# Performance work log

Measured on AMD Instinct MI355X. Metric: run time of the kernel, lower is better.

The kernel has to match this reference:

```python
import jax, jax.numpy as jnp
import numpy as np

B, N = 262144, 32
NEG = -1e4  # acts as -inf: exp(NEG) == 0 in fp32, clean gradients (softmax weight 0)


def setup_inputs() -> dict:
    key = jax.random.key(0)
    k1, k2, k3 = jax.random.split(key, 3)
    scores = jax.random.normal(k1, (B, N), dtype=jnp.float32)
    ranks = jax.random.randint(k2, (B, N), 0, 32, dtype=jnp.int64)
    mask = jax.random.randint(k3, (B, N), 0, 2, dtype=jnp.int32).astype(bool)
    return {"scores": scores, "ranks": ranks, "mask": mask}


def reference(scores, ranks, mask):
    # n valid (non-padded) items per row
    n = jnp.sum(~mask, axis=1)                              # [B]
    # sort each row by rank, pushing padded entries to the end (stable sort,
    # matching per-row argsort over the valid subset in the original)
    sort_key = jnp.where(mask, N + 1, ranks)                # [B, N]
    order = jnp.argsort(sort_key, axis=1)                   # jnp argsort is stable
    s_sorted = jnp.take_along_axis(scores, order, axis=1)   # [B, N]

    pos = jnp.arange(N)
    valid = pos[None, :] < n[:, None]                       # first n slots hold valid scores
    s_m = jnp.where(valid, s_sorted, NEG)                   # padded -> effectively -inf

    # reverse cumulative logsumexp: rev_lse[k] = logsumexp(s_sorted[k:n])
    rev_lse = jax.lax.cumlogsumexp(s_m, axis=1, reverse=True)

    # original sums k = 0 .. n-2 of -(s_k - logsumexp(s_{k:}))
    term_mask = pos[None, :] < (n[:, None] - 1)
    per_row = -jnp.sum(jnp.where(term_mask, s_m - rev_lse, 0.0), axis=1)  # [B]

    use = n >= 2                                            # rows with < 2 valid are skipped
    per_row = jnp.where(use, per_row / jnp.maximum(n, 1).astype(per_row.dtype), 0.0)
    n_valid = jnp.sum(use)
    return jnp.sum(per_row) / jnp.maximum(n_valid, 1).astype(per_row.dtype)
```

## Files before the change

kernel.cpp:

```cpp
#include <hip/hip_runtime.h>
#include <cstdint>

#define TPB 256
#define LOG2E 1.4426950408889634f
#define LN2   0.69314718055994531f

__global__ __launch_bounds__(TPB, 4)
void pl_main(const float* __restrict__ scores,
             const int* __restrict__ ranks,
             const int* __restrict__ mask,
             float* __restrict__ partials,
             int B)
{
    const int tid = threadIdx.x;
    const int row = blockIdx.x * TPB + tid;

    __shared__ float eb[32 * TPB];

    float per_row = 0.0f, cnt = 0.0f;

    if (row < B) {
        const float4* sp = reinterpret_cast<const float4*>(scores) + (size_t)row * 8;
        const int4*   rp = reinterpret_cast<const int4*>(ranks)  + (size_t)row * 8;
        const int4*   mp = reinterpret_cast<const int4*>(mask)   + (size_t)row * 8;

        float4 sv[8];
        #pragma unroll
        for (int c = 0; c < 8; ++c) sv[c] = sp[c];

        unsigned K[32];
        int nm = 0;
        #pragma unroll
        for (int c = 0; c < 8; ++c) {
            const int4 rv = rp[c];
            const int4 qv = mp[c];
            const int j = c * 4;
            K[j+0] = (unsigned)((qv.x << 10) + (rv.x << 5) + (j+0));
            K[j+1] = (unsigned)((qv.y << 10) + (rv.y << 5) + (j+1));
            K[j+2] = (unsigned)((qv.z << 10) + (rv.z << 5) + (j+2));
            K[j+3] = (unsigned)((qv.w << 10) + (rv.w << 5) + (j+3));
            nm += (qv.x + qv.y) + (qv.z + qv.w);
        }
        const int n = 32 - nm;

        #pragma unroll
        for (int kk = 2; kk <= 32; kk <<= 1) {
            #pragma unroll
            for (int jj = kk >> 1; jj > 0; jj >>= 1) {
                #pragma unroll
                for (int i = 0; i < 32; ++i) {
                    const int l = i ^ jj;
                    if (l > i) {
                        const unsigned a = K[i], b = K[l];
                        const unsigned mn = a < b ? a : b;
                        const unsigned mh = a < b ? b : a;
                        if ((i & kk) == 0) { K[i] = mn; K[l] = mh; }
                        else               { K[i] = mh; K[l] = mn; }
                    }
                }
            }
        }

        float cm[8];
        #pragma unroll
        for (int c = 0; c < 8; ++c)
            cm[c] = fmaxf(fmaxf(sv[c].x, sv[c].y), fmaxf(sv[c].z, sv[c].w));
        const float mx = fmaxf(fmaxf(fmaxf(cm[0], cm[1]), fmaxf(cm[2], cm[3])),
                               fmaxf(fmaxf(cm[4], cm[5]), fmaxf(cm[6], cm[7])));
        const float nml = -mx * LOG2E;

        #pragma unroll
        for (int c = 0; c < 8; ++c) {
            const int j = c * 4;
            eb[(j+0)*TPB + tid] = __builtin_amdgcn_exp2f(__builtin_fmaf(sv[c].x, LOG2E, nml));
            eb[(j+1)*TPB + tid] = __builtin_amdgcn_exp2f(__builtin_fmaf(sv[c].y, LOG2E, nml));
            eb[(j+2)*TPB + tid] = __builtin_amdgcn_exp2f(__builtin_fmaf(sv[c].z, LOG2E, nml));
            eb[(j+3)*TPB + tid] = __builtin_amdgcn_exp2f(__builtin_fmaf(sv[c].w, LOG2E, nml));
        }

        float es[32];
        #pragma unroll
        for (int p = 0; p < 32; ++p)
            es[p] = eb[(K[p] & 31u) * TPB + tid];

        float t = 0.0f, lsum = 0.0f;
        #pragma unroll
        for (int g = 7; g >= 0; --g) {
            float pT = 1.0f, pE = 1.0f;
            #pragma unroll
            for (int q = 3; q >= 0; --q) {
                const int p = 4*g + q;
                const bool v = (p < n);
                t  += v ? es[p] : 0.0f;
                pT *= v ? t     : 1.0f;
                pE *= v ? es[p] : 1.0f;
            }
            lsum += __builtin_amdgcn_logf(pT) - __builtin_amdgcn_logf(pE);
        }

        if (n >= 2) {
            per_row = (LN2 * lsum) / (float)n;
            cnt = 1.0f;
        }
    }

    #pragma unroll
    for (int d = 32; d >= 1; d >>= 1) {
        per_row += __shfl_xor(per_row, d, 64);
        cnt     += __shfl_xor(cnt,     d, 64);
    }
    __shared__ float rbuf[8];
    if ((tid & 63) == 0) {
        rbuf[(tid >> 6)]     = per_row;
        rbuf[4 + (tid >> 6)] = cnt;
    }
    __syncthreads();
    if (tid == 0) {
        partials[2*blockIdx.x]     = (rbuf[0] + rbuf[1]) + (rbuf[2] + rbuf[3]);
        partials[2*blockIdx.x + 1] = (rbuf[4] + rbuf[5]) + (rbuf[6] + rbuf[7]);
    }
}

__global__ __launch_bounds__(256)
void pl_final(const float* __restrict__ partials, int nb, float* __restrict__ out)
{
    const int tid = threadIdx.x;
    float s = 0.0f, c = 0.0f;
    for (int i = tid; i < nb; i += 256) {
        s += partials[2*i];
        c += partials[2*i + 1];
    }
    #pragma unroll
    for (int d = 32; d >= 1; d >>= 1) {
        s += __shfl_xor(s, d, 64);
        c += __shfl_xor(c, d, 64);
    }
    __shared__ float sb[8];
    if ((tid & 63) == 0) {
        sb[tid >> 6]       = s;
        sb[4 + (tid >> 6)] = c;
    }
    __syncthreads();
    if (tid == 0) {
        const float S = sb[0] + sb[1] + sb[2] + sb[3];
        const float C = sb[4] + sb[5] + sb[6] + sb[7];
        out[0] = S / fmaxf(C, 1.0f);
    }
}

extern "C" void kernel_launch(void* const* d_in, const int* in_sizes, int n_in,
                              void* d_out, int out_size, void* d_ws, size_t ws_size,
                              hipStream_t stream)
{
    const float* scores = (const float*)d_in[0];
    const int*   ranks  = (const int*)d_in[1];
    const int*   mask   = (const int*)d_in[2];

    const int B  = in_sizes[0] / 32;
    const int nb = (B + TPB - 1) / TPB;

    float* partials = (float*)d_ws;

    pl_main<<<nb, TPB, 0, stream>>>(scores, ranks, mask, partials, B);
    pl_final<<<1, 256, 0, stream>>>(partials, nb, (float*)d_out);
}
```

Before: 27.07 us.

## Pack bf16 exp values with sort keys and stage coalesced loads through LDS

Loads for the block's tile are now coalesced across threads and staged through shared memory, replacing per-thread strided row loads. Each element's exp(score) is rounded to bf16 and packed into the low 16 bits of the 32-bit sort key, so the bitonic sort carries the values with it and the separate exp buffer and gather are removed. Validity and the count n come from the key bits instead of a separate reduction. The max subtraction before exp is dropped, which risks bf16 precision loss and overflow or underflow for large scores, and adds a block barrier.

```diff
diff --git a/kernel.cpp b/kernel.cpp
--- a/kernel.cpp
+++ b/kernel.cpp
@@ -4,6 +4,8 @@
 #define TPB 256
 #define LOG2E 1.4426950408889634f
 #define LN2   0.69314718055994531f
+#define RS    36
+#define VALID_LIM (1024u << 16)
 
 __global__ __launch_bounds__(TPB, 4)
 void pl_main(const float* __restrict__ scores,
@@ -13,35 +15,66 @@
              int B)
 {
     const int tid = threadIdx.x;
+
+    __shared__ unsigned pb[TPB * RS];
+
+    const size_t tile4 = (size_t)blockIdx.x * (TPB * 8);
+    const size_t tot4  = (size_t)B * 8;
+
+    const float4* sp = reinterpret_cast<const float4*>(scores) + tile4;
+    const int4*   rp = reinterpret_cast<const int4*>(ranks)   + tile4;
+    const int4*   mp = reinterpret_cast<const int4*>(mask)    + tile4;
+
+    #pragma unroll
+    for (int i = 0; i < 8; ++i) {
+        const int f = i * TPB + tid;
+        if (tile4 + f < tot4) {
+            const float4 sv = sp[f];
+            const int4   rv = rp[f];
+            const int4   qv = mp[f];
+            const int rowL = f >> 3;
+            const int j0   = (f & 7) * 4;
+
+            uint4 w;
+            {
+                const float e = __builtin_amdgcn_exp2f(sv.x * LOG2E);
+                const unsigned b = __builtin_bit_cast(unsigned, e);
+                const unsigned b16 = (b + 0x7FFFu + ((b >> 16) & 1u)) >> 16;
+                w.x = ((unsigned)((qv.x << 10) + (rv.x << 5) + (j0 + 0)) << 16) | b16;
+            }
+            {
+                const float e = __builtin_amdgcn_exp2f(sv.y * LOG2E);
+                const unsigned b = __builtin_bit_cast(unsigned, e);
+                const unsigned b16 = (b + 0x7FFFu + ((b >> 16) & 1u)) >> 16;
+                w.y = ((unsigned)((qv.y << 10) + (rv.y << 5) + (j0 + 1)) << 16) | b16;
+            }
+            {
+                const float e = __builtin_amdgcn_exp2f(sv.z * LOG2E);
+                const unsigned b = __builtin_bit_cast(unsigned, e);
+                const unsigned b16 = (b + 0x7FFFu + ((b >> 16) & 1u)) >> 16;
+                w.z = ((unsigned)((qv.z << 10) + (rv.z << 5) + (j0 + 2)) << 16) | b16;
+            }
+            {
+                const float e = __builtin_amdgcn_exp2f(sv.w * LOG2E);
+                const unsigned b = __builtin_bit_cast(unsigned, e);
+                const unsigned b16 = (b + 0x7FFFu + ((b >> 16) & 1u)) >> 16;
+                w.w = ((unsigned)((qv.w << 10) + (rv.w << 5) + (j0 + 3)) << 16) | b16;
+            }
+            *reinterpret_cast<uint4*>(&pb[rowL * RS + j0]) = w;
+        }
+    }
+    __syncthreads();
+
+    float per_row = 0.0f, cnt = 0.0f;
     const int row = blockIdx.x * TPB + tid;
 
-    __shared__ float eb[32 * TPB];
-
-    float per_row = 0.0f, cnt = 0.0f;
-
     if (row < B) {
-        const float4* sp = reinterpret_cast<const float4*>(scores) + (size_t)row * 8;
-        const int4*   rp = reinterpret_cast<const int4*>(ranks)  + (size_t)row * 8;
-        const int4*   mp = reinterpret_cast<const int4*>(mask)   + (size_t)row * 8;
-
-        float4 sv[8];
-        #pragma unroll
-        for (int c = 0; c < 8; ++c) sv[c] = sp[c];
-
-        unsigned K[32];
-        int nm = 0;
+        unsigned U[32];
         #pragma unroll
         for (int c = 0; c < 8; ++c) {
-            const int4 rv = rp[c];
-            const int4 qv = mp[c];
-            const int j = c * 4;
-            K[j+0] = (unsigned)((qv.x << 10) + (rv.x << 5) + (j+0));
-            K[j+1] = (unsigned)((qv.y << 10) + (rv.y << 5) + (j+1));
-            K[j+2] = (unsigned)((qv.z << 10) + (rv.z << 5) + (j+2));
-            K[j+3] = (unsigned)((qv.w << 10) + (rv.w << 5) + (j+3));
-            nm += (qv.x + qv.y) + (qv.z + qv.w);
+            const uint4 v = *reinterpret_cast<const uint4*>(&pb[tid * RS + c * 4]);
+            U[c*4+0] = v.x; U[c*4+1] = v.y; U[c*4+2] = v.z; U[c*4+3] = v.w;
         }
-        const int n = 32 - nm;
 
         #pragma unroll
         for (int kk = 2; kk <= 32; kk <<= 1) {
@@ -51,38 +84,17 @@
                 for (int i = 0; i < 32; ++i) {
                     const int l = i ^ jj;
                     if (l > i) {
-                        const unsigned a = K[i], b = K[l];
+                        const unsigned a = U[i], b = U[l];
                         const unsigned mn = a < b ? a : b;
                         const unsigned mh = a < b ? b : a;
-                        if ((i & kk) == 0) { K[i] = mn; K[l] = mh; }
-                        else               { K[i] = mh; K[l] = mn; }
+                        if ((i & kk) == 0) { U[i] = mn; U[l] = mh; }
+                        else               { U[i] = mh; U[l] = mn; }
                     }
                 }
             }
         }
 
-        float cm[8];
-        #pragma unroll
-        for (int c = 0; c < 8; ++c)
-            cm[c] = fmaxf(fmaxf(sv[c].x, sv[c].y), fmaxf(sv[c].z, sv[c].w));
-        const float mx = fmaxf(fmaxf(fmaxf(cm[0], cm[1]), fmaxf(cm[2], cm[3])),
-                               fmaxf(fmaxf(cm[4], cm[5]), fmaxf(cm[6], cm[7])));
-        const float nml = -mx * LOG2E;
-
-        #pragma unroll
-        for (int c = 0; c < 8; ++c) {
-            const int j = c * 4;
-            eb[(j+0)*TPB + tid] = __builtin_amdgcn_exp2f(__builtin_fmaf(sv[c].x, LOG2E, nml));
-            eb[(j+1)*TPB + tid] = __builtin_amdgcn_exp2f(__builtin_fmaf(sv[c].y, LOG2E, nml));
-            eb[(j+2)*TPB + tid] = __builtin_amdgcn_exp2f(__builtin_fmaf(sv[c].z, LOG2E, nml));
-            eb[(j+3)*TPB + tid] = __builtin_amdgcn_exp2f(__builtin_fmaf(sv[c].w, LOG2E, nml));
-        }
-
-        float es[32];
-        #pragma unroll
-        for (int p = 0; p < 32; ++p)
-            es[p] = eb[(K[p] & 31u) * TPB + tid];
-
+        int   n = 0;
         float t = 0.0f, lsum = 0.0f;
         #pragma unroll
         for (int g = 7; g >= 0; --g) {
@@ -90,10 +102,12 @@
             #pragma unroll
             for (int q = 3; q >= 0; --q) {
                 const int p = 4*g + q;
-                const bool v = (p < n);
-                t  += v ? es[p] : 0.0f;
-                pT *= v ? t     : 1.0f;
-                pE *= v ? es[p] : 1.0f;
+                const bool v = (U[p] < VALID_LIM);
+                const float e = __builtin_bit_cast(float, U[p] << 16);
+                n  += v ? 1 : 0;
+                t  += v ? e : 0.0f;
+                pT *= v ? t : 1.0f;
+                pE *= v ? e : 1.0f;
             }
             lsum += __builtin_amdgcn_logf(pT) - __builtin_amdgcn_logf(pE);
         }
```

New measurement: 28.69 us. +6.0%, slower.
